# Optimization experiments

Hardware: AMD Instinct MI355X
Metric: run time of the kernel (lower is better)

## Reference

```python
import jax, jax.numpy as jnp
import numpy as np

K, D = 1024, 256
B, H, W = 16, 64, 64


def setup_inputs() -> dict:
    key = jax.random.key(0)
    k1, k2 = jax.random.split(key)
    z_e_x = jax.random.normal(k1, (B, D, H, W), dtype=jnp.float32)
    # nn.Embedding weight initialized uniform(-1/K, 1/K)
    embedding = jax.random.uniform(k2, (K, D), dtype=jnp.float32,
                                   minval=-1.0 / K, maxval=1.0 / K)
    return {"z_e_x": z_e_x, "embedding": embedding}


def reference(z_e_x, embedding):
    # permute(0,2,3,1): [B,D,H,W] -> [B,H,W,D]
    z = jnp.transpose(z_e_x, (0, 2, 3, 1))
    flat = z.reshape(-1, z.shape[-1])  # [N, D], N = B*H*W
    # squared L2 distances: ||z||^2 - 2 z.e + ||e||^2  -> [N, K]
    dists = (jnp.sum(flat * flat, axis=1, keepdims=True)
             - 2.0 * flat @ embedding.T
             + jnp.sum(embedding * embedding, axis=1))
    indices = jnp.argmin(dists, axis=1)  # [N]
    # vq() returns latents with the spatial shape [B, H, W]
    return indices.reshape(z.shape[:-1]).astype(jnp.int32)
```

## Files before the change

### kernel.cpp

```cpp
#include <hip/hip_runtime.h>


#define D_DIM  256
#define K_DIM  1024
#define HW     4096
#define N_TOT  65536
#define NSPLIT 8
#define KSPL   (K_DIM / NSPLIT)
#define KT     32
#define NKT    (KSPL / KT)
#define F32MAX 3.402823466e38f


__global__ void ee_kernel(const float* __restrict__ e, float* __restrict__ ee) {
#pragma clang fp contract(off)
    int k = blockIdx.x * blockDim.x + threadIdx.x;
    if (k >= K_DIM) return;
    const float* row = e + (size_t)k * D_DIM;
    float total = 0.0f;
    #pragma unroll
    for (int h = 0; h < 2; ++h) {
        const float* a = row + h * 128;
        float r[8];
        #pragma unroll
        for (int j = 0; j < 8; ++j) { float v = a[j]; r[j] = v * v; }
        #pragma unroll
        for (int i = 8; i < 128; i += 8) {
            #pragma unroll
            for (int j = 0; j < 8; ++j) { float v = a[i + j]; r[j] = r[j] + v * v; }
        }
        float s = ((r[0] + r[1]) + (r[2] + r[3])) + ((r[4] + r[5]) + (r[6] + r[7]));
        total = (h == 0) ? s : (total + s);
    }
    ee[k] = total;
}

__global__ void a_kernel(const float* __restrict__ z, float* __restrict__ A) {
#pragma clang fp contract(off)
    int n = blockIdx.x * blockDim.x + threadIdx.x;
    int b  = n >> 12;
    int hw = n & (HW - 1);
    const float* base = z + (size_t)b * D_DIM * HW + hw;
    float total = 0.0f;
    #pragma unroll
    for (int h = 0; h < 2; ++h) {
        float r[8];
        #pragma unroll
        for (int j = 0; j < 8; ++j) {
            float v = base[(size_t)(h * 128 + j) * HW];
            r[j] = v * v;
        }
        #pragma unroll
        for (int i = 8; i < 128; i += 8) {
            #pragma unroll
            for (int j = 0; j < 8; ++j) {
                float v = base[(size_t)(h * 128 + i + j) * HW];
                r[j] = r[j] + v * v;
            }
        }
        float s = ((r[0] + r[1]) + (r[2] + r[3])) + ((r[4] + r[5]) + (r[6] + r[7]));
        total = (h == 0) ? s : (total + s);
    }
    A[n] = total;
}


__global__ void pack_kernel(const float* __restrict__ e, float* __restrict__ epk) {
    int k = blockIdx.x;
    int d = threadIdx.x;
    int s  = k >> 7;
    int kt = (k >> 5) & (NKT - 1);
    int j  = k & (KT - 1);
    epk[(((size_t)(s * NKT + kt) * D_DIM + d) * KT) + j] = 2.0f * e[(size_t)k * D_DIM + d];
}


__launch_bounds__(256, 4)
__global__ void vq_partial(const float* __restrict__ z, const float* __restrict__ epk,
                           const float* __restrict__ A, const float* __restrict__ ee,
                           float* __restrict__ pv, int* __restrict__ pk) {
#pragma clang fp contract(off)
    const int tid  = threadIdx.x;
    const int s    = blockIdx.x & (NSPLIT - 1);
    const int slab = blockIdx.x >> 3;
    const int n0   = slab * 512 + tid;
    const int n1   = n0 + 256;
    const int b    = n0 >> 12;
    const float* __restrict__ zp0 = z + (size_t)b * D_DIM * HW + (n0 & (HW - 1));
    const float* __restrict__ zp1 = z + (size_t)b * D_DIM * HW + (n1 & (HW - 1));
    const float* __restrict__ ebase = epk + (size_t)s * (NKT * D_DIM * KT);

    const float An0 = A[n0];
    const float An1 = A[n1];
    float best0 = F32MAX, best1 = F32MAX;
    int   bk0 = 0, bk1 = 0;

    float za0[8], za1[8], zb0[8], zb1[8];
    #pragma unroll
    for (int i = 0; i < 8; ++i) {
        za0[i] = zp0[(size_t)i * HW];
        za1[i] = zp1[(size_t)i * HW];
    }

    #pragma unroll 1
    for (int kt = 0; kt < NKT; ++kt) {
        const float* __restrict__ ek = ebase + (size_t)kt * (D_DIM * KT);
        float a0[KT], a1[KT];
        #pragma unroll
        for (int j = 0; j < KT; ++j) { a0[j] = 0.0f; a1[j] = 0.0f; }

        #pragma unroll 1
        for (int it = 0; it < 16; ++it) {
            const int base = it * 16;
            #pragma unroll
            for (int i = 0; i < 8; ++i) {
                const size_t idx = (size_t)((base + 8 + i) & (D_DIM - 1)) * HW;
                zb0[i] = zp0[idx];
                zb1[i] = zp1[idx];
            }
            #pragma unroll
            for (int dd = 0; dd < 8; ++dd) {
                const float zv0 = za0[dd], zv1 = za1[dd];
                const float* __restrict__ er = ek + (size_t)(base + dd) * KT;
                #pragma unroll
                for (int j = 0; j < KT; ++j) {
                    const float ev = er[j];
                    a0[j] = fmaf(zv0, ev, a0[j]);
                    a1[j] = fmaf(zv1, ev, a1[j]);
                }
            }
            #pragma unroll
            for (int i = 0; i < 8; ++i) {
                const size_t idx = (size_t)((base + 16 + i) & (D_DIM - 1)) * HW;
                za0[i] = zp0[idx];
                za1[i] = zp1[idx];
            }
            #pragma unroll
            for (int dd = 0; dd < 8; ++dd) {
                const float zv0 = zb0[dd], zv1 = zb1[dd];
                const float* __restrict__ er = ek + (size_t)(base + 8 + dd) * KT;
                #pragma unroll
                for (int j = 0; j < KT; ++j) {
                    const float ev = er[j];
                    a0[j] = fmaf(zv0, ev, a0[j]);
                    a1[j] = fmaf(zv1, ev, a1[j]);
                }
            }
        }

        const int kbase = s * KSPL + kt * KT;
        #pragma unroll
        for (int j = 0; j < KT; ++j) {
            const int kg = kbase + j;
            const float eev = ee[kg];
            const float d0 = (An0 - a0[j]) + eev;
            const float d1 = (An1 - a1[j]) + eev;
            if (d0 < best0) { best0 = d0; bk0 = kg; }
            if (d1 < best1) { best1 = d1; bk1 = kg; }
        }
    }

    pv[(size_t)s * N_TOT + n0] = best0;
    pk[(size_t)s * N_TOT + n0] = bk0;
    pv[(size_t)s * N_TOT + n1] = best1;
    pk[(size_t)s * N_TOT + n1] = bk1;
}


__global__ void combine_kernel(const float* __restrict__ pv, const int* __restrict__ pk,
                               int* __restrict__ out) {
    int n = blockIdx.x * blockDim.x + threadIdx.x;
    float bv = pv[n];
    int   bk = pk[n];
    #pragma unroll
    for (int s2 = 1; s2 < NSPLIT; ++s2) {
        float v = pv[(size_t)s2 * N_TOT + n];
        int   k = pk[(size_t)s2 * N_TOT + n];
        if (v < bv) { bv = v; bk = k; }
    }
    out[n] = bk;
}

extern "C" void kernel_launch(void* const* d_in, const int* in_sizes, int n_in,
                              void* d_out, int out_size, void* d_ws, size_t ws_size,
                              hipStream_t stream) {
    const float* z   = (const float*)d_in[0];
    const float* emb = (const float*)d_in[1];
    int* out = (int*)d_out;

    float* wsA   = (float*)d_ws;
    float* wsEE  = wsA + N_TOT;
    float* wsEPK = wsEE + K_DIM;
    float* wsPV  = wsEPK + (size_t)D_DIM * K_DIM;
    int*   wsPK  = (int*)(wsPV + (size_t)NSPLIT * N_TOT);

    pack_kernel<<<K_DIM, 256, 0, stream>>>(emb, wsEPK);
    ee_kernel<<<K_DIM / 256, 256, 0, stream>>>(emb, wsEE);
    a_kernel<<<N_TOT / 256, 256, 0, stream>>>(z, wsA);
    vq_partial<<<(N_TOT / 512) * NSPLIT, 256, 0, stream>>>(z, wsEPK, wsA, wsEE, wsPV, wsPK);
    combine_kernel<<<N_TOT / 256, 256, 0, stream>>>(wsPV, wsPK, out);
}
```

Before: 518.9 us.

## Stage codebook tiles in LDS with wider K tile and merge prep kernels

The main distance kernel now copies each 64-code slice of the packed, doubled codebook into shared memory with float4 loads and reads it back as float4 broadcasts, replacing per-thread global/scalar loads. KT grows from 32 to 64, so each thread keeps 128 accumulators, and launch bounds drop to 2 blocks per CU to leave room for the registers. The pack, codebook-norm and z-norm kernels are fused into one launch to save launch overhead. The costs are lower occupancy, 64 KB of LDS per block, and a block barrier for every K tile.

```diff
diff --git a/kernel.cpp b/kernel.cpp
--- a/kernel.cpp
+++ b/kernel.cpp
@@ -7,79 +7,79 @@
 #define N_TOT  65536
 #define NSPLIT 8
 #define KSPL   (K_DIM / NSPLIT)
-#define KT     32
+#define KT     64
 #define NKT    (KSPL / KT)
 #define F32MAX 3.402823466e38f
 
 
-__global__ void ee_kernel(const float* __restrict__ e, float* __restrict__ ee) {
+__global__ void prep_kernel(const float* __restrict__ e, const float* __restrict__ z,
+                            float* __restrict__ epk, float* __restrict__ ee,
+                            float* __restrict__ A) {
 #pragma clang fp contract(off)
-    int k = blockIdx.x * blockDim.x + threadIdx.x;
-    if (k >= K_DIM) return;
-    const float* row = e + (size_t)k * D_DIM;
-    float total = 0.0f;
-    #pragma unroll
-    for (int h = 0; h < 2; ++h) {
-        const float* a = row + h * 128;
-        float r[8];
-        #pragma unroll
-        for (int j = 0; j < 8; ++j) { float v = a[j]; r[j] = v * v; }
-        #pragma unroll
-        for (int i = 8; i < 128; i += 8) {
-            #pragma unroll
-            for (int j = 0; j < 8; ++j) { float v = a[i + j]; r[j] = r[j] + v * v; }
-        }
-        float s = ((r[0] + r[1]) + (r[2] + r[3])) + ((r[4] + r[5]) + (r[6] + r[7]));
-        total = (h == 0) ? s : (total + s);
-    }
-    ee[k] = total;
-}
-
-__global__ void a_kernel(const float* __restrict__ z, float* __restrict__ A) {
+    const int bid = blockIdx.x;
+    const int tid = threadIdx.x;
+
+    if (bid < 1024) {
+        const int k = bid, d = tid;
+        epk[((size_t)(k >> 6) * D_DIM + d) * KT + (k & 63)] = 2.0f * e[(size_t)k * D_DIM + d];
+        return;
+    }
+    if (bid < 1028) {
+        const int k = (bid - 1024) * 256 + tid;
+        const float* row = e + (size_t)k * D_DIM;
+        float total = 0.0f;
+        #pragma unroll
+        for (int h = 0; h < 2; ++h) {
+            const float* a = row + h * 128;
+            float r[8];
+            #pragma unroll
+            for (int j = 0; j < 8; ++j) { float v = a[j]; r[j] = v * v; }
+            #pragma unroll
+            for (int i = 8; i < 128; i += 8) {
+                #pragma unroll
+                for (int j = 0; j < 8; ++j) { float v = a[i + j]; r[j] = r[j] + v * v; }
+            }
+            float s = ((r[0] + r[1]) + (r[2] + r[3])) + ((r[4] + r[5]) + (r[6] + r[7]));
+            total = (h == 0) ? s : (total + s);
+        }
+        ee[k] = total;
+        return;
+    }
+    {
+        const int n = (bid - 1028) * 256 + tid;
+        const float* base = z + (size_t)(n >> 12) * D_DIM * HW + (n & (HW - 1));
+        float total = 0.0f;
+        #pragma unroll
+        for (int h = 0; h < 2; ++h) {
+            float r[8];
+            #pragma unroll
+            for (int j = 0; j < 8; ++j) {
+                float v = base[(size_t)(h * 128 + j) * HW];
+                r[j] = v * v;
+            }
+            #pragma unroll
+            for (int i = 8; i < 128; i += 8) {
+                #pragma unroll
+                for (int j = 0; j < 8; ++j) {
+                    float v = base[(size_t)(h * 128 + i + j) * HW];
+                    r[j] = r[j] + v * v;
+                }
+            }
+            float s = ((r[0] + r[1]) + (r[2] + r[3])) + ((r[4] + r[5]) + (r[6] + r[7]));
+            total = (h == 0) ? s : (total + s);
+        }
+        A[n] = total;
+    }
+}
+
+
+__launch_bounds__(256, 2)
+__global__ void vq_main(const float* __restrict__ z, const float* __restrict__ epk,
+                        const float* __restrict__ A, const float* __restrict__ ee,
+                        float* __restrict__ pv, int* __restrict__ pk) {
 #pragma clang fp contract(off)
-    int n = blockIdx.x * blockDim.x + threadIdx.x;
-    int b  = n >> 12;
-    int hw = n & (HW - 1);
-    const float* base = z + (size_t)b * D_DIM * HW + hw;
-    float total = 0.0f;
-    #pragma unroll
-    for (int h = 0; h < 2; ++h) {
-        float r[8];
-        #pragma unroll
-        for (int j = 0; j < 8; ++j) {
-            float v = base[(size_t)(h * 128 + j) * HW];
-            r[j] = v * v;
-        }
-        #pragma unroll
-        for (int i = 8; i < 128; i += 8) {
-            #pragma unroll
-            for (int j = 0; j < 8; ++j) {
-                float v = base[(size_t)(h * 128 + i + j) * HW];
-                r[j] = r[j] + v * v;
-            }
-        }
-        float s = ((r[0] + r[1]) + (r[2] + r[3])) + ((r[4] + r[5]) + (r[6] + r[7]));
-        total = (h == 0) ? s : (total + s);
-    }
-    A[n] = total;
-}
-
-
-__global__ void pack_kernel(const float* __restrict__ e, float* __restrict__ epk) {
-    int k = blockIdx.x;
-    int d = threadIdx.x;
-    int s  = k >> 7;
-    int kt = (k >> 5) & (NKT - 1);
-    int j  = k & (KT - 1);
-    epk[(((size_t)(s * NKT + kt) * D_DIM + d) * KT) + j] = 2.0f * e[(size_t)k * D_DIM + d];
-}
-
-
-__launch_bounds__(256, 4)
-__global__ void vq_partial(const float* __restrict__ z, const float* __restrict__ epk,
-                           const float* __restrict__ A, const float* __restrict__ ee,
-                           float* __restrict__ pv, int* __restrict__ pk) {
-#pragma clang fp contract(off)
+    __shared__ __align__(16) float es[D_DIM * KT];
+
     const int tid  = threadIdx.x;
     const int s    = blockIdx.x & (NSPLIT - 1);
     const int slab = blockIdx.x >> 3;
@@ -88,7 +88,6 @@
     const int b    = n0 >> 12;
     const float* __restrict__ zp0 = z + (size_t)b * D_DIM * HW + (n0 & (HW - 1));
     const float* __restrict__ zp1 = z + (size_t)b * D_DIM * HW + (n1 & (HW - 1));
-    const float* __restrict__ ebase = epk + (size_t)s * (NKT * D_DIM * KT);
 
     const float An0 = A[n0];
     const float An1 = A[n1];
@@ -104,7 +103,17 @@
 
     #pragma unroll 1
     for (int kt = 0; kt < NKT; ++kt) {
-        const float* __restrict__ ek = ebase + (size_t)kt * (D_DIM * KT);
+        __syncthreads();
+        {
+            const float* __restrict__ eg = epk + (size_t)(2 * s + kt) * (D_DIM * KT);
+            #pragma unroll
+            for (int r = 0; r < 16; ++r) {
+                const int f = (r * 256 + tid) * 4;
+                *(float4*)&es[f] = *(const float4*)(eg + f);
+            }
+        }
+        __syncthreads();
+
         float a0[KT], a1[KT];
         #pragma unroll
         for (int j = 0; j < KT; ++j) { a0[j] = 0.0f; a1[j] = 0.0f; }
@@ -121,12 +130,19 @@
             #pragma unroll
             for (int dd = 0; dd < 8; ++dd) {
                 const float zv0 = za0[dd], zv1 = za1[dd];
-                const float* __restrict__ er = ek + (size_t)(base + dd) * KT;
-                #pragma unroll
-                for (int j = 0; j < KT; ++j) {
-                    const float ev = er[j];
-                    a0[j] = fmaf(zv0, ev, a0[j]);
-                    a1[j] = fmaf(zv1, ev, a1[j]);
+                const float4* __restrict__ e4 = (const float4*)&es[(base + dd) * KT];
+                #pragma unroll
+                for (int q = 0; q < 16; ++q) {
+                    const float4 ev = e4[q];
+                    const int j = q * 4;
+                    a0[j+0] = fmaf(zv0, ev.x, a0[j+0]);
+                    a1[j+0] = fmaf(zv1, ev.x, a1[j+0]);
+                    a0[j+1] = fmaf(zv0, ev.y, a0[j+1]);
+                    a1[j+1] = fmaf(zv1, ev.y, a1[j+1]);
+                    a0[j+2] = fmaf(zv0, ev.z, a0[j+2]);
+                    a1[j+2] = fmaf(zv1, ev.z, a1[j+2]);
+                    a0[j+3] = fmaf(zv0, ev.w, a0[j+3]);
+                    a1[j+3] = fmaf(zv1, ev.w, a1[j+3]);
                 }
             }
             #pragma unroll
@@ -138,20 +154,27 @@
             #pragma unroll
             for (int dd = 0; dd < 8; ++dd) {
                 const float zv0 = zb0[dd], zv1 = zb1[dd];
-                const float* __restrict__ er = ek + (size_t)(base + 8 + dd) * KT;
-                #pragma unroll
-                for (int j = 0; j < KT; ++j) {
-                    const float ev = er[j];
-                    a0[j] = fmaf(zv0, ev, a0[j]);
-                    a1[j] = fmaf(zv1, ev, a1[j]);
+                const float4* __restrict__ e4 = (const float4*)&es[(base + 8 + dd) * KT];
+                #pragma unroll
+                for (int q = 0; q < 16; ++q) {
+                    const float4 ev = e4[q];
+                    const int j = q * 4;
+                    a0[j+0] = fmaf(zv0, ev.x, a0[j+0]);
+                    a1[j+0] = fmaf(zv1, ev.x, a1[j+0]);
+                    a0[j+1] = fmaf(zv0, ev.y, a0[j+1]);
+                    a1[j+1] = fmaf(zv1, ev.y, a1[j+1]);
+                    a0[j+2] = fmaf(zv0, ev.z, a0[j+2]);
+                    a1[j+2] = fmaf(zv1, ev.z, a1[j+2]);
+                    a0[j+3] = fmaf(zv0, ev.w, a0[j+3]);
+                    a1[j+3] = fmaf(zv1, ev.w, a1[j+3]);
                 }
             }
         }
 
-        const int kbase = s * KSPL + kt * KT;
+        const int kb = s * KSPL + kt * KT;
         #pragma unroll
         for (int j = 0; j < KT; ++j) {
-            const int kg = kbase + j;
+            const int kg = kb + j;
             const float eev = ee[kg];
             const float d0 = (An0 - a0[j]) + eev;
             const float d1 = (An1 - a1[j]) + eev;
@@ -194,9 +217,7 @@
     float* wsPV  = wsEPK + (size_t)D_DIM * K_DIM;
     int*   wsPK  = (int*)(wsPV + (size_t)NSPLIT * N_TOT);
 
-    pack_kernel<<<K_DIM, 256, 0, stream>>>(emb, wsEPK);
-    ee_kernel<<<K_DIM / 256, 256, 0, stream>>>(emb, wsEE);
-    a_kernel<<<N_TOT / 256, 256, 0, stream>>>(z, wsA);
-    vq_partial<<<(N_TOT / 512) * NSPLIT, 256, 0, stream>>>(z, wsEPK, wsA, wsEE, wsPV, wsPK);
+    prep_kernel<<<1284, 256, 0, stream>>>(emb, z, wsEPK, wsEE, wsA);
+    vq_main<<<(N_TOT / 512) * NSPLIT, 256, 0, stream>>>(z, wsEPK, wsA, wsEE, wsPV, wsPK);
     combine_kernel<<<N_TOT / 256, 256, 0, stream>>>(wsPV, wsPK, out);
 }
```

Result: slower. 1.538 ms (+196.5%).
